# Performance work log

Hardware: AMD Instinct MI355X
Metric: run time of the kernel (lower is better)

## Reference

```python
import jax, jax.numpy as jnp
import numpy as np

H = 512   # hidden_size
E = 256   # embedding_size
V = 32000 # vocab_size
L = 1024  # max_length (encoder seq len)
B = 64    # batch


def setup_inputs() -> dict:
    key = jax.random.key(0)
    ks = jax.random.split(key, 18)
    n = lambda i, shape, s=0.05: (jax.random.normal(ks[i], shape, dtype=jnp.float32) * s)
    return {
        "input": jax.random.randint(ks[0], (B, 1), 0, V),
        "last_output_context": n(1, (1, B, H), 1.0),
        "last_hidden": n(2, (1, B, H), 1.0),
        "last_cell_state": n(3, (1, B, H), 1.0),
        "encoder_outputs": n(4, (L, B, H), 1.0),
        "emb": n(5, (V, E)),
        "W_ih": n(6, (4 * H, E + H)),
        "W_hh": n(7, (4 * H, H)),
        "b_ih": n(8, (4 * H,)),
        "b_hh": n(9, (4 * H,)),
        "W_attn": n(10, (H, 2 * H)),
        "b_attn": n(11, (H,)),
        "beta": n(12, (H, 1), 1.0),
        "W_oc": n(13, (H, 2 * H)),
        "b_oc": n(14, (H,)),
        "W_out": n(15, (V, H)),
        "b_out": n(16, (V,)),
    }


def reference(input, last_output_context, last_hidden, last_cell_state,
              encoder_outputs, emb, W_ih, W_hh, b_ih, b_hh,
              W_attn, b_attn, beta, W_oc, b_oc, W_out, b_out):
    # embedding lookup: (B,1) -> (B,E)  (permute(1,0,2) then squeeze step dim)
    tok = emb[input[:, 0]]                                   # (B, E)
    x = jnp.concatenate([tok, last_output_context[0]], axis=1)  # (B, E+H)
    # single-step LSTM (PyTorch gate order i, f, g, o)
    gates = x @ W_ih.T + last_hidden[0] @ W_hh.T + b_ih + b_hh  # (B, 4H)
    i_g, f_g, g_g, o_g = jnp.split(gates, 4, axis=1)
    i_g = jax.nn.sigmoid(i_g)
    f_g = jax.nn.sigmoid(f_g)
    g_g = jnp.tanh(g_g)
    o_g = jax.nn.sigmoid(o_g)
    c = f_g * last_cell_state[0] + i_g * g_g                  # (B, H)
    h = o_g * jnp.tanh(c)                                     # (B, H) == rnn_output
    # additive attention, vectorized over the seq_len loop
    h_tiled = jnp.broadcast_to(h[None], (L, B, H))
    cat = jnp.concatenate([h_tiled, encoder_outputs], axis=-1)  # (L, B, 2H)
    energy = jnp.tanh(cat @ W_attn.T + b_attn) @ beta           # (L, B, 1)
    attn_w = jax.nn.softmax(energy[..., 0], axis=0)             # (L, B) softmax over seq
    # context = bmm(attn_weights, encoder_outputs)
    context = jnp.einsum('lb,lbh->bh', attn_w, encoder_outputs)  # (B, H)
    co = jnp.tanh(jnp.concatenate([h, context], axis=1) @ W_oc.T + b_oc)  # (B, H)
    output = jax.nn.log_softmax(co @ W_out.T + b_out, axis=1)    # (B, V)
    return output, co[None], h[None], c[None]
```

## Files before the change

kernel.cpp:

```cpp
#include <hip/hip_runtime.h>
#include <hip/hip_bf16.h>
#include <cstddef>

#define H   512
#define E   256
#define V   32000
#define L   1024
#define B   64
#define KX  768
#define M_TOT 65536

typedef __attribute__((ext_vector_type(8))) _Float16 half8v;
typedef __attribute__((ext_vector_type(4))) float f32x4;

__device__ __forceinline__ half8v cvt8(float4 x0, float4 x1) {
    union { half8v v; _Float16 u[8]; } hv;
    hv.u[0] = (_Float16)x0.x; hv.u[1] = (_Float16)x0.y;
    hv.u[2] = (_Float16)x0.z; hv.u[3] = (_Float16)x0.w;
    hv.u[4] = (_Float16)x1.x; hv.u[5] = (_Float16)x1.y;
    hv.u[6] = (_Float16)x1.z; hv.u[7] = (_Float16)x1.w;
    return hv.v;
}

__device__ __forceinline__ void glds16(const unsigned short* g, unsigned short* l) {
    __builtin_amdgcn_global_load_lds(
        (const __attribute__((address_space(1))) void*)g,
        (__attribute__((address_space(3))) void*)l, 16, 0, 0);
}

__global__ __launch_bounds__(256) void k_conv_enc(const float* __restrict__ enc,
                                                  unsigned short* __restrict__ encT) {
    size_t u = (size_t)blockIdx.x * 256 + threadIdx.x;
    int s = (int)(u & 3);
    size_t rowg = u >> 2;
    int row = (int)(rowg & 127);
    size_t mtkt = rowg >> 7;
    int kt = (int)(mtkt & 15);
    size_t mt = mtkt >> 4;
    const float* src = &enc[(mt * 128 + row) * 512 + kt * 32 + s * 8];
    float4 x0 = *reinterpret_cast<const float4*>(src);
    float4 x1 = *reinterpret_cast<const float4*>(src + 4);
    *reinterpret_cast<half8v*>(&encT[u * 8]) = cvt8(x0, x1);
}

__global__ __launch_bounds__(256) void k_conv_w2(const float* __restrict__ W_attn,
                                                 unsigned short* __restrict__ WfT) {
    int u = blockIdx.x * 256 + threadIdx.x;
    int s = u & 3;
    int rowg = u >> 2;
    int row = rowg & 127;
    int jtkt = rowg >> 7;
    int kt = jtkt & 15;
    int jt = jtkt >> 4;
    int j = jt * 128 + row;
    const float* src = &W_attn[(size_t)j * (2 * H) + H + kt * 32 + s * 8];
    float4 x0 = *reinterpret_cast<const float4*>(src);
    float4 x1 = *reinterpret_cast<const float4*>(src + 4);
    *reinterpret_cast<half8v*>(&WfT[u * 8]) = cvt8(x0, x1);
}

__global__ __launch_bounds__(256) void k_build(const int* __restrict__ inp,
                                               const float* __restrict__ loc,
                                               const float* __restrict__ hprev,
                                               const float* __restrict__ emb,
                                               float* __restrict__ xprevT) {
    int gid = blockIdx.x * 256 + threadIdx.x;
    int k = gid >> 6, b = gid & 63;
    float v;
    if (k < 256)      v = emb[(size_t)inp[b] * E + k];
    else if (k < 768) v = loc[b * H + (k - 256)];
    else              v = hprev[b * H + (k - 768)];
    xprevT[gid] = v;
}

__global__ __launch_bounds__(256) void k_lstm(const float* __restrict__ W_ih,
                                              const float* __restrict__ W_hh,
                                              const float* __restrict__ b_ih,
                                              const float* __restrict__ b_hh,
                                              const float* __restrict__ xprevT,
                                              const float* __restrict__ cprev,
                                              float* __restrict__ h_out,
                                              float* __restrict__ c_out,
                                              float* __restrict__ hnewT) {
    int u = blockIdx.x;
    int w = threadIdx.x >> 6;
    int b = threadIdx.x & 63;
    int j = w * 512 + u;
    float a0 = 0.f, a1 = 0.f, a2 = 0.f, a3 = 0.f;
    const float* Wr = &W_ih[(size_t)j * KX];
    for (int k = 0; k < KX; k += 4) {
        float4 wv = *reinterpret_cast<const float4*>(&Wr[k]);
        a0 += wv.x * xprevT[(k + 0) * 64 + b];
        a1 += wv.y * xprevT[(k + 1) * 64 + b];
        a2 += wv.z * xprevT[(k + 2) * 64 + b];
        a3 += wv.w * xprevT[(k + 3) * 64 + b];
    }
    const float* Wr2 = &W_hh[(size_t)j * H];
    const float* hT = &xprevT[KX * 64];
    for (int k = 0; k < H; k += 4) {
        float4 wv = *reinterpret_cast<const float4*>(&Wr2[k]);
        a0 += wv.x * hT[(k + 0) * 64 + b];
        a1 += wv.y * hT[(k + 1) * 64 + b];
        a2 += wv.z * hT[(k + 2) * 64 + b];
        a3 += wv.w * hT[(k + 3) * 64 + b];
    }
    float acc = b_ih[j] + b_hh[j] + ((a0 + a1) + (a2 + a3));
    __shared__ float gs[4][64];
    gs[w][b] = acc;
    __syncthreads();
    if (threadIdx.x < 64) {
        float ig = 1.f / (1.f + __expf(-gs[0][b]));
        float fg = 1.f / (1.f + __expf(-gs[1][b]));
        float gg = tanhf(gs[2][b]);
        float og = 1.f / (1.f + __expf(-gs[3][b]));
        float c = fg * cprev[b * H + u] + ig * gg;
        float h = og * tanhf(c);
        c_out[b * H + u] = c;
        h_out[b * H + u] = h;
        hnewT[u * 64 + b] = h;
    }
}

__global__ __launch_bounds__(256) void k_hw(const float* __restrict__ W_attn,
                                            const float* __restrict__ b_attn,
                                            const float* __restrict__ hT,
                                            float* __restrict__ hW_jb) {
    int j = blockIdx.x * 4 + (threadIdx.x >> 6);
    int b = threadIdx.x & 63;
    float a0 = 0.f, a1 = 0.f, a2 = 0.f, a3 = 0.f;
    const float* Wr = &W_attn[(size_t)j * (2 * H)];
    for (int k = 0; k < H; k += 4) {
        float4 wv = *reinterpret_cast<const float4*>(&Wr[k]);
        a0 += wv.x * hT[(k + 0) * 64 + b];
        a1 += wv.y * hT[(k + 1) * 64 + b];
        a2 += wv.z * hT[(k + 2) * 64 + b];
        a3 += wv.w * hT[(k + 3) * 64 + b];
    }
    hW_jb[j * 64 + b] = b_attn[j] + ((a0 + a1) + (a2 + a3));
}

__global__ __launch_bounds__(256, 4) void k_energy_v9(
        const unsigned short* __restrict__ encT,
        const unsigned short* __restrict__ WfT,
        const float* __restrict__ hW,
        const float* __restrict__ beta,
        float* __restrict__ partial_e) {
    __shared__ unsigned short Ah[128 * 32];
    __shared__ unsigned short Bh[128 * 32];
    __shared__ float red[2][128];

    const int tid  = threadIdx.x;
    const int lane = tid & 63;
    const int w    = tid >> 6;
    const int wm = w >> 1;
    const int wn = w & 1;
    const int bid = blockIdx.x;
    const int xcd = bid & 7;
    const int loc = bid >> 3;
    const int mt  = xcd * 64 + (loc >> 2);
    const int jt  = loc & 3;
    const int m0 = mt * 128;
    const int j0 = jt * 128;

    const unsigned short* Ag = encT + (size_t)mt * (16 * 4096) + w * 1024 + lane * 8;
    const unsigned short* Bg = WfT  + (size_t)jt * (16 * 4096) + w * 1024 + lane * 8;
    unsigned short* Al = &Ah[w * 1024];
    unsigned short* Bl = &Bh[w * 1024];

    f32x4 acc[4][4];
    #pragma unroll
    for (int i = 0; i < 4; ++i)
        #pragma unroll
        for (int j = 0; j < 4; ++j) acc[i][j] = (f32x4){0.f, 0.f, 0.f, 0.f};

    const int fr = lane & 15;
    const int s8 = (lane >> 4) * 8;

    for (int kt = 0; kt < 16; ++kt) {
        const int g0 = kt * 4096;
        glds16(Ag + g0,       Al);
        glds16(Ag + g0 + 512, Al + 512);
        glds16(Bg + g0,       Bl);
        glds16(Bg + g0 + 512, Bl + 512);
        __syncthreads();
        half8v a_h[4], b_h[4];
        #pragma unroll
        for (int mf = 0; mf < 4; ++mf)
            a_h[mf] = *reinterpret_cast<const half8v*>(
                &Ah[(wm * 64 + mf * 16 + fr) * 32 + s8]);
        #pragma unroll
        for (int nf = 0; nf < 4; ++nf)
            b_h[nf] = *reinterpret_cast<const half8v*>(
                &Bh[(wn * 64 + nf * 16 + fr) * 32 + s8]);
        #pragma unroll
        for (int mf = 0; mf < 4; ++mf)
            #pragma unroll
            for (int nf = 0; nf < 4; ++nf)
                acc[mf][nf] = __builtin_amdgcn_mfma_f32_16x16x32_f16(
                    a_h[mf], b_h[nf], acc[mf][nf], 0, 0, 0);
        __syncthreads();
    }

    float psum[4][4];
    #pragma unroll
    for (int i = 0; i < 4; ++i)
        #pragma unroll
        for (int r = 0; r < 4; ++r) psum[i][r] = 0.f;
    #pragma unroll
    for (int nf = 0; nf < 4; ++nf) {
        int jj = j0 + wn * 64 + nf * 16 + (lane & 15);
        float bet = beta[jj];
        #pragma unroll
        for (int mf = 0; mf < 4; ++mf) {
            int b_base = (wm * 64 + mf * 16 + (lane >> 4) * 4) & 63;
            float4 hw4 = *reinterpret_cast<const float4*>(&hW[jj * 64 + b_base]);
            float hwv[4] = {hw4.x, hw4.y, hw4.z, hw4.w};
            #pragma unroll
            for (int r = 0; r < 4; ++r) {
                float e = acc[mf][nf][r] + hwv[r];
                float ex = __expf(2.f * e);
                psum[mf][r] += bet * (1.f - 2.f / (ex + 1.f));
            }
        }
    }
    #pragma unroll
    for (int mf = 0; mf < 4; ++mf)
        #pragma unroll
        for (int r = 0; r < 4; ++r) {
            float v = psum[mf][r];
            v += __shfl_xor(v, 1);
            v += __shfl_xor(v, 2);
            v += __shfl_xor(v, 4);
            v += __shfl_xor(v, 8);
            psum[mf][r] = v;
        }
    __syncthreads();
    if ((lane & 15) == 0) {
        #pragma unroll
        for (int mf = 0; mf < 4; ++mf)
            #pragma unroll
            for (int r = 0; r < 4; ++r)
                red[wn][wm * 64 + mf * 16 + (lane >> 4) * 4 + r] = psum[mf][r];
    }
    __syncthreads();
    if (tid < 128)
        partial_e[(size_t)jt * M_TOT + m0 + tid] = red[0][tid] + red[1][tid];
}

__global__ __launch_bounds__(256) void k_softmax_l(const float* __restrict__ partial_e,
                                                   float* __restrict__ attn_w) {
    int b = blockIdx.x;
    int tid = threadIdx.x;
    float el[4];
    float m = -1e30f;
    #pragma unroll
    for (int i = 0; i < 4; ++i) {
        int l = i * 256 + tid;
        float e = 0.f;
        #pragma unroll
        for (int nb = 0; nb < 4; ++nb)
            e += partial_e[(size_t)nb * M_TOT + l * 64 + b];
        el[i] = e;
        m = fmaxf(m, e);
    }
    #pragma unroll
    for (int s = 1; s < 64; s <<= 1) m = fmaxf(m, __shfl_xor(m, s));
    __shared__ float redm[4];
    if ((tid & 63) == 0) redm[tid >> 6] = m;
    __syncthreads();
    m = fmaxf(fmaxf(redm[0], redm[1]), fmaxf(redm[2], redm[3]));
    float s = 0.f;
    #pragma unroll
    for (int i = 0; i < 4; ++i) { el[i] = __expf(el[i] - m); s += el[i]; }
    #pragma unroll
    for (int sh = 1; sh < 64; sh <<= 1) s += __shfl_xor(s, sh);
    __shared__ float reds[4];
    if ((tid & 63) == 0) reds[tid >> 6] = s;
    __syncthreads();
    s = reds[0] + reds[1] + reds[2] + reds[3];
    float inv = 1.f / s;
    #pragma unroll
    for (int i = 0; i < 4; ++i)
        attn_w[(i * 256 + tid) * 64 + b] = el[i] * inv;
}

__global__ __launch_bounds__(128) void k_ctx_part(const float* __restrict__ attn_w,
                                                  const float* __restrict__ enc,
                                                  float* __restrict__ ctx_part) {
    int chunk = blockIdx.x, b = blockIdx.y;
    int h = threadIdx.x * 4;
    float4 acc = {0.f, 0.f, 0.f, 0.f};
    for (int i = 0; i < 32; ++i) {
        int l = chunk * 32 + i;
        float w = attn_w[l * 64 + b];
        float4 e4 = *reinterpret_cast<const float4*>(
            &enc[((size_t)l * 64 + b) * H + h]);
        acc.x += w * e4.x;
        acc.y += w * e4.y;
        acc.z += w * e4.z;
        acc.w += w * e4.w;
    }
    *reinterpret_cast<float4*>(&ctx_part[((size_t)(chunk * 64 + b)) * H + h]) = acc;
}

__global__ __launch_bounds__(256) void k_ctx_reduce(const float* __restrict__ ctx_part,
                                                    float* __restrict__ ctxT) {
    int gid = blockIdx.x * 256 + threadIdx.x;
    int b = gid >> 9, h = gid & 511;
    float s = 0.f;
    for (int c = 0; c < 32; ++c)
        s += ctx_part[((size_t)(c * 64 + b)) * H + h];
    ctxT[h * 64 + b] = s;
}

__global__ __launch_bounds__(256) void k_co(const float* __restrict__ W_oc,
                                            const float* __restrict__ b_oc,
                                            const float* __restrict__ hT,
                                            const float* __restrict__ ctxT,
                                            float* __restrict__ co_out) {
    int j = blockIdx.x * 4 + (threadIdx.x >> 6);
    int b = threadIdx.x & 63;
    float a0 = 0.f, a1 = 0.f, a2 = 0.f, a3 = 0.f;
    const float* Wr = &W_oc[(size_t)j * (2 * H)];
    for (int k = 0; k < H; k += 4) {
        float4 wv = *reinterpret_cast<const float4*>(&Wr[k]);
        a0 += wv.x * hT[(k + 0) * 64 + b];
        a1 += wv.y * hT[(k + 1) * 64 + b];
        a2 += wv.z * hT[(k + 2) * 64 + b];
        a3 += wv.w * hT[(k + 3) * 64 + b];
    }
    const float* Wr2 = Wr + H;
    for (int k = 0; k < H; k += 4) {
        float4 wv = *reinterpret_cast<const float4*>(&Wr2[k]);
        a0 += wv.x * ctxT[(k + 0) * 64 + b];
        a1 += wv.y * ctxT[(k + 1) * 64 + b];
        a2 += wv.z * ctxT[(k + 2) * 64 + b];
        a3 += wv.w * ctxT[(k + 3) * 64 + b];
    }
    co_out[b * H + j] = tanhf(b_oc[j] + ((a0 + a1) + (a2 + a3)));
}

__global__ __launch_bounds__(256) void k_logits_v3(const float* __restrict__ co,
                                                   const float* __restrict__ W_out,
                                                   const float* __restrict__ b_out,
                                                   float* __restrict__ logits) {
    const int tid  = threadIdx.x;
    const int lane = tid & 63;
    const int w    = tid >> 6;
    const int fr   = lane & 15;
    const int kb   = (lane >> 4) * 8;
    const int j    = blockIdx.x * 64 + w * 16 + fr;

    f32x4 acc[4];
    #pragma unroll
    for (int mf = 0; mf < 4; ++mf) acc[mf] = (f32x4){0.f, 0.f, 0.f, 0.f};

    const float* Arow = &co[(size_t)fr * H + kb];
    const float* Brow = &W_out[(size_t)j * H + kb];

    for (int k0 = 0; k0 < H; k0 += 32) {
        float4 b0 = *reinterpret_cast<const float4*>(Brow + k0);
        float4 b1 = *reinterpret_cast<const float4*>(Brow + k0 + 4);
        half8v bh = cvt8(b0, b1);
        #pragma unroll
        for (int mf = 0; mf < 4; ++mf) {
            const float* ap = Arow + (size_t)mf * 16 * H + k0;
            float4 a0 = *reinterpret_cast<const float4*>(ap);
            float4 a1 = *reinterpret_cast<const float4*>(ap + 4);
            half8v ah = cvt8(a0, a1);
            acc[mf] = __builtin_amdgcn_mfma_f32_16x16x32_f16(ah, bh, acc[mf], 0, 0, 0);
        }
    }
    float bo = b_out[j];
    #pragma unroll
    for (int mf = 0; mf < 4; ++mf) {
        int mbase = mf * 16 + (lane >> 4) * 4;
        #pragma unroll
        for (int r = 0; r < 4; ++r)
            logits[(size_t)(mbase + r) * V + j] = acc[mf][r] + bo;
    }
}

__global__ __launch_bounds__(256) void k_lsm_part(const float* __restrict__ logits,
                                                  float* __restrict__ pmax,
                                                  float* __restrict__ psum) {
    int chunk = blockIdx.x, b = blockIdx.y;
    int tid = threadIdx.x;
    const float* row = &logits[(size_t)b * V + chunk * 4000];
    float v[16];
    float m = -1e30f;
    #pragma unroll
    for (int t = 0; t < 16; ++t) {
        int i = t * 256 + tid;
        v[t] = (i < 4000) ? row[i] : -1e30f;
        m = fmaxf(m, v[t]);
    }
    #pragma unroll
    for (int s = 1; s < 64; s <<= 1) m = fmaxf(m, __shfl_xor(m, s));
    __shared__ float redm[4];
    if ((tid & 63) == 0) redm[tid >> 6] = m;
    __syncthreads();
    m = fmaxf(fmaxf(redm[0], redm[1]), fmaxf(redm[2], redm[3]));
    float s = 0.f;
    #pragma unroll
    for (int t = 0; t < 16; ++t) s += __expf(v[t] - m);
    #pragma unroll
    for (int sh = 1; sh < 64; sh <<= 1) s += __shfl_xor(s, sh);
    __shared__ float reds[4];
    if ((tid & 63) == 0) reds[tid >> 6] = s;
    __syncthreads();
    if (tid == 0) {
        pmax[chunk * 64 + b] = m;
        psum[chunk * 64 + b] = reds[0] + reds[1] + reds[2] + reds[3];
    }
}

__global__ __launch_bounds__(64) void k_lsm_final(const float* __restrict__ pmax,
                                                  const float* __restrict__ psum,
                                                  float* __restrict__ lse) {
    int b = threadIdx.x;
    float m = -1e30f;
    #pragma unroll
    for (int c = 0; c < 8; ++c) m = fmaxf(m, pmax[c * 64 + b]);
    float s = 0.f;
    #pragma unroll
    for (int c = 0; c < 8; ++c) s += psum[c * 64 + b] * __expf(pmax[c * 64 + b] - m);
    lse[b] = m + __logf(s);
}

__global__ __launch_bounds__(256) void k_lsm_write(const float* __restrict__ logits,
                                                   const float* __restrict__ lse,
                                                   float* __restrict__ out) {
    size_t i4 = ((size_t)blockIdx.x * 256 + threadIdx.x) * 4;
    int b = (int)(i4 / V);
    float l = lse[b];
    float4 x = *reinterpret_cast<const float4*>(&logits[i4]);
    x.x -= l; x.y -= l; x.z -= l; x.w -= l;
    *reinterpret_cast<float4*>(&out[i4]) = x;
}

extern "C" void kernel_launch(void* const* d_in, const int* in_sizes, int n_in,
                              void* d_out, int out_size, void* d_ws, size_t ws_size,
                              hipStream_t stream) {
    const int*   inp    = (const int*)  d_in[0];
    const float* loc    = (const float*)d_in[1];
    const float* hprev  = (const float*)d_in[2];
    const float* cprev  = (const float*)d_in[3];
    const float* enc    = (const float*)d_in[4];
    const float* emb    = (const float*)d_in[5];
    const float* W_ih   = (const float*)d_in[6];
    const float* W_hh   = (const float*)d_in[7];
    const float* b_ih   = (const float*)d_in[8];
    const float* b_hh   = (const float*)d_in[9];
    const float* W_attn = (const float*)d_in[10];
    const float* b_attn = (const float*)d_in[11];
    const float* beta   = (const float*)d_in[12];
    const float* W_oc   = (const float*)d_in[13];
    const float* b_oc   = (const float*)d_in[14];
    const float* W_out  = (const float*)d_in[15];
    const float* b_out  = (const float*)d_in[16];

    float* out = (float*)d_out;
    float* out_co = out + (size_t)B * V;
    float* out_h  = out_co + B * H;
    float* out_c  = out_h  + B * H;

    float* ws = (float*)d_ws;
    float* xprevT = ws;
    float* hnewT  = xprevT + 1280 * 64;
    float* hW     = hnewT  + H * 64;
    float* pe     = hW     + H * 64;
    float* attnw  = pe     + 4 * M_TOT;
    float* ctxp   = attnw  + M_TOT;
    float* ctxT   = ctxp   + 32 * 64 * H;
    float* logits = ctxT   + H * 64;
    float* pmax   = logits + (size_t)B * V;
    float* psum   = pmax   + 512;
    float* lse    = psum   + 512;
    unsigned short* WfT  = (unsigned short*)(lse + 64);
    unsigned short* encT = WfT + (size_t)H * H;

    k_conv_w2<<<128, 256, 0, stream>>>(W_attn, WfT);
    k_build <<<320, 256, 0, stream>>>(inp, loc, hprev, emb, xprevT);
    k_lstm  <<<512, 256, 0, stream>>>(W_ih, W_hh, b_ih, b_hh, xprevT, cprev,
                                      out_h, out_c, hnewT);
    k_hw    <<<128, 256, 0, stream>>>(W_attn, b_attn, hnewT, hW);
    k_conv_enc<<<16384, 256, 0, stream>>>(enc, encT);
    k_energy_v9<<<2048, 256, 0, stream>>>(encT, WfT, hW, beta, pe);
    k_softmax_l<<<64, 256, 0, stream>>>(pe, attnw);
    k_ctx_part <<<dim3(32, 64), 128, 0, stream>>>(attnw, enc, ctxp);
    k_ctx_reduce<<<128, 256, 0, stream>>>(ctxp, ctxT);
    k_co    <<<128, 256, 0, stream>>>(W_oc, b_oc, hnewT, ctxT, out_co);
    k_logits_v3<<<500, 256, 0, stream>>>(out_co, W_out, b_out, logits);
    k_lsm_part<<<dim3(8, 64), 256, 0, stream>>>(logits, pmax, psum);
    k_lsm_final<<<1, 64, 0, stream>>>(pmax, psum, lse);
    k_lsm_write<<<2000, 256, 0, stream>>>(logits, lse, out);
}
```

Before: 292.2 us.

## Swizzle fp16 tile layout, double K-step per stage, read fp16 encoder in context kernel

Rewrites the fp16 conversion of encoder outputs and W_attn into 128x64 K-tiles with an XOR swizzle on 8-element groups, so LDS reads avoid bank conflicts. The energy GEMM now loads 64-wide K slabs, halving the number of barriers and load rounds per tile. The context kernel reads the fp16 swizzled encoder copy instead of the fp32 original, halving its global traffic. The cost is that the context sum now uses fp16-rounded encoder values, which changes precision, and it uses more LDS per block, which may limit occupancy.

```diff
diff --git a/kernel.cpp b/kernel.cpp
--- a/kernel.cpp
+++ b/kernel.cpp
@@ -28,35 +28,35 @@
         (__attribute__((address_space(3))) void*)l, 16, 0, 0);
 }
 
+
 __global__ __launch_bounds__(256) void k_conv_enc(const float* __restrict__ enc,
                                                   unsigned short* __restrict__ encT) {
     size_t u = (size_t)blockIdx.x * 256 + threadIdx.x;
-    int s = (int)(u & 3);
-    size_t rowg = u >> 2;
-    int row = (int)(rowg & 127);
-    size_t mtkt = rowg >> 7;
-    int kt = (int)(mtkt & 15);
-    size_t mt = mtkt >> 4;
-    const float* src = &enc[(mt * 128 + row) * 512 + kt * 32 + s * 8];
+    size_t m = u >> 6;
+    int g = (int)(u & 63);
+    int kt2 = g >> 3, s = g & 7;
+    int r = (int)(m & 127);
+    size_t mt = m >> 7;
+    const float* src = &enc[m * 512 + kt2 * 64 + s * 8];
     float4 x0 = *reinterpret_cast<const float4*>(src);
     float4 x1 = *reinterpret_cast<const float4*>(src + 4);
-    *reinterpret_cast<half8v*>(&encT[u * 8]) = cvt8(x0, x1);
+    size_t dst = (((mt * 8 + kt2) * 128 + r) * 64) + (size_t)((s ^ (r & 7)) * 8);
+    *reinterpret_cast<half8v*>(&encT[dst]) = cvt8(x0, x1);
 }
 
 __global__ __launch_bounds__(256) void k_conv_w2(const float* __restrict__ W_attn,
                                                  unsigned short* __restrict__ WfT) {
     int u = blockIdx.x * 256 + threadIdx.x;
-    int s = u & 3;
-    int rowg = u >> 2;
-    int row = rowg & 127;
-    int jtkt = rowg >> 7;
-    int kt = jtkt & 15;
-    int jt = jtkt >> 4;
-    int j = jt * 128 + row;
-    const float* src = &W_attn[(size_t)j * (2 * H) + H + kt * 32 + s * 8];
+    int j = u >> 6;
+    int g = u & 63;
+    int kt2 = g >> 3, s = g & 7;
+    int r = j & 127;
+    int jt = j >> 7;
+    const float* src = &W_attn[(size_t)j * (2 * H) + H + kt2 * 64 + s * 8];
     float4 x0 = *reinterpret_cast<const float4*>(src);
     float4 x1 = *reinterpret_cast<const float4*>(src + 4);
-    *reinterpret_cast<half8v*>(&WfT[u * 8]) = cvt8(x0, x1);
+    int dst = ((jt * 8 + kt2) * 128 + r) * 64 + ((s ^ (r & 7)) * 8);
+    *reinterpret_cast<half8v*>(&WfT[dst]) = cvt8(x0, x1);
 }
 
 __global__ __launch_bounds__(256) void k_build(const int* __restrict__ inp,
@@ -139,14 +139,14 @@
     hW_jb[j * 64 + b] = b_attn[j] + ((a0 + a1) + (a2 + a3));
 }
 
-__global__ __launch_bounds__(256, 4) void k_energy_v9(
+__global__ __launch_bounds__(256, 4) void k_energy_v10(
         const unsigned short* __restrict__ encT,
         const unsigned short* __restrict__ WfT,
         const float* __restrict__ hW,
         const float* __restrict__ beta,
         float* __restrict__ partial_e) {
-    __shared__ unsigned short Ah[128 * 32];
-    __shared__ unsigned short Bh[128 * 32];
+    __shared__ unsigned short Ah[128 * 64];
+    __shared__ unsigned short Bh[128 * 64];
     __shared__ float red[2][128];
 
     const int tid  = threadIdx.x;
@@ -162,10 +162,10 @@
     const int m0 = mt * 128;
     const int j0 = jt * 128;
 
-    const unsigned short* Ag = encT + (size_t)mt * (16 * 4096) + w * 1024 + lane * 8;
-    const unsigned short* Bg = WfT  + (size_t)jt * (16 * 4096) + w * 1024 + lane * 8;
-    unsigned short* Al = &Ah[w * 1024];
-    unsigned short* Bl = &Bh[w * 1024];
+    const unsigned short* Ag = encT + (size_t)mt * (8 * 8192) + w * 2048 + lane * 8;
+    const unsigned short* Bg = WfT  + (size_t)jt * (8 * 8192) + w * 2048 + lane * 8;
+    unsigned short* Al = &Ah[w * 2048];
+    unsigned short* Bl = &Bh[w * 2048];
 
     f32x4 acc[4][4];
     #pragma unroll
@@ -174,30 +174,38 @@
         for (int j = 0; j < 4; ++j) acc[i][j] = (f32x4){0.f, 0.f, 0.f, 0.f};
 
     const int fr = lane & 15;
-    const int s8 = (lane >> 4) * 8;
-
-    for (int kt = 0; kt < 16; ++kt) {
-        const int g0 = kt * 4096;
-        glds16(Ag + g0,       Al);
-        glds16(Ag + g0 + 512, Al + 512);
-        glds16(Bg + g0,       Bl);
-        glds16(Bg + g0 + 512, Bl + 512);
+    const int g  = lane >> 4;
+
+    for (int kt2 = 0; kt2 < 8; ++kt2) {
+        const int g0 = kt2 * 8192;
+        glds16(Ag + g0,        Al);
+        glds16(Ag + g0 + 512,  Al + 512);
+        glds16(Ag + g0 + 1024, Al + 1024);
+        glds16(Ag + g0 + 1536, Al + 1536);
+        glds16(Bg + g0,        Bl);
+        glds16(Bg + g0 + 512,  Bl + 512);
+        glds16(Bg + g0 + 1024, Bl + 1024);
+        glds16(Bg + g0 + 1536, Bl + 1536);
         __syncthreads();
-        half8v a_h[4], b_h[4];
-        #pragma unroll
-        for (int mf = 0; mf < 4; ++mf)
-            a_h[mf] = *reinterpret_cast<const half8v*>(
-                &Ah[(wm * 64 + mf * 16 + fr) * 32 + s8]);
-        #pragma unroll
-        for (int nf = 0; nf < 4; ++nf)
-            b_h[nf] = *reinterpret_cast<const half8v*>(
-                &Bh[(wn * 64 + nf * 16 + fr) * 32 + s8]);
-        #pragma unroll
-        for (int mf = 0; mf < 4; ++mf)
+        #pragma unroll
+        for (int kh = 0; kh < 2; ++kh) {
+            const int sp = ((kh * 4 + g) ^ (fr & 7)) * 8;
+            half8v a_h[4], b_h[4];
+            #pragma unroll
+            for (int mf = 0; mf < 4; ++mf)
+                a_h[mf] = *reinterpret_cast<const half8v*>(
+                    &Ah[(wm * 64 + mf * 16 + fr) * 64 + sp]);
             #pragma unroll
             for (int nf = 0; nf < 4; ++nf)
-                acc[mf][nf] = __builtin_amdgcn_mfma_f32_16x16x32_f16(
-                    a_h[mf], b_h[nf], acc[mf][nf], 0, 0, 0);
+                b_h[nf] = *reinterpret_cast<const half8v*>(
+                    &Bh[(wn * 64 + nf * 16 + fr) * 64 + sp]);
+            #pragma unroll
+            for (int mf = 0; mf < 4; ++mf)
+                #pragma unroll
+                for (int nf = 0; nf < 4; ++nf)
+                    acc[mf][nf] = __builtin_amdgcn_mfma_f32_16x16x32_f16(
+                        a_h[mf], b_h[nf], acc[mf][nf], 0, 0, 0);
+        }
         __syncthreads();
     }
 
@@ -284,23 +292,29 @@
         attn_w[(i * 256 + tid) * 64 + b] = el[i] * inv;
 }
 
-__global__ __launch_bounds__(128) void k_ctx_part(const float* __restrict__ attn_w,
-                                                  const float* __restrict__ enc,
-                                                  float* __restrict__ ctx_part) {
+__global__ __launch_bounds__(64) void k_ctx_part(const float* __restrict__ attn_w,
+                                                 const unsigned short* __restrict__ encT,
+                                                 float* __restrict__ ctx_part) {
     int chunk = blockIdx.x, b = blockIdx.y;
-    int h = threadIdx.x * 4;
-    float4 acc = {0.f, 0.f, 0.f, 0.f};
+    int t = threadIdx.x;
+    int kt2 = t >> 3, s = t & 7;
+    float acc[8];
+    #pragma unroll
+    for (int i = 0; i < 8; ++i) acc[i] = 0.f;
     for (int i = 0; i < 32; ++i) {
         int l = chunk * 32 + i;
+        int m = l * 64 + b;
         float w = attn_w[l * 64 + b];
-        float4 e4 = *reinterpret_cast<const float4*>(
-            &enc[((size_t)l * 64 + b) * H + h]);
-        acc.x += w * e4.x;
-        acc.y += w * e4.y;
-        acc.z += w * e4.z;
-        acc.w += w * e4.w;
-    }
-    *reinterpret_cast<float4*>(&ctx_part[((size_t)(chunk * 64 + b)) * H + h]) = acc;
+        int r = m & 127;
+        size_t mt = (size_t)(m >> 7);
+        size_t addr = ((mt * 8 + kt2) * 128 + r) * 64 + (size_t)((s ^ (r & 7)) * 8);
+        half8v hv = *reinterpret_cast<const half8v*>(&encT[addr]);
+        #pragma unroll
+        for (int q = 0; q < 8; ++q) acc[q] += w * (float)hv[q];
+    }
+    float* dst = &ctx_part[((size_t)(chunk * 64 + b)) * H + t * 8];
+    #pragma unroll
+    for (int q = 0; q < 8; ++q) dst[q] = acc[q];
 }
 
 __global__ __launch_bounds__(256) void k_ctx_reduce(const float* __restrict__ ctx_part,
@@ -486,9 +500,9 @@
                                       out_h, out_c, hnewT);
     k_hw    <<<128, 256, 0, stream>>>(W_attn, b_attn, hnewT, hW);
     k_conv_enc<<<16384, 256, 0, stream>>>(enc, encT);
-    k_energy_v9<<<2048, 256, 0, stream>>>(encT, WfT, hW, beta, pe);
+    k_energy_v10<<<2048, 256, 0, stream>>>(encT, WfT, hW, beta, pe);
     k_softmax_l<<<64, 256, 0, stream>>>(pe, attnw);
-    k_ctx_part <<<dim3(32, 64), 128, 0, stream>>>(attnw, enc, ctxp);
+    k_ctx_part <<<dim3(32, 64), 64, 0, stream>>>(attnw, encT, ctxp);
     k_ctx_reduce<<<128, 256, 0, stream>>>(ctxp, ctxT);
     k_co    <<<128, 256, 0, stream>>>(W_oc, b_oc, hnewT, ctxT, out_co);
     k_logits_v3<<<500, 256, 0, stream>>>(out_co, W_out, b_out, logits);
```

Result: faster. 282.5 us (-3.3%).
